# Kernel tuning notes

Hardware: AMD Instinct MI355X
Metric: run time of the kernel (lower is better)

Reference implementation:

```python
import jax, jax.numpy as jnp
import numpy as np

B, L, C = 2, 4096, 1024
H, WIN = 16, 128            # num_heads, window_size (each side)
D = C // H                  # head_dim = 64


def setup_inputs() -> dict:
    key = jax.random.key(0)
    ks = jax.random.split(key, 9)
    s = 0.02
    return {
        "x": jax.random.normal(ks[0], (B, L, C), jnp.float32),
        # Linear weights stored as [in, out] (y = x @ W + b), same math as torch Linear.
        "wq": jax.random.normal(ks[1], (C, C), jnp.float32) * s,
        "bq": jnp.zeros((C,), jnp.float32),
        "wk": jax.random.normal(ks[2], (C, C), jnp.float32) * s,
        "bk": jnp.zeros((C,), jnp.float32),
        "wv": jax.random.normal(ks[3], (C, C), jnp.float32) * s,
        "bv": jnp.zeros((C,), jnp.float32),
        "wo": jax.random.normal(ks[4], (C, C), jnp.float32) * s,
        "bo": jnp.zeros((C,), jnp.float32),
    }


def reference(x, wq, bq, wk, bk, wv, bv, wo, bo):
    b, l, c = x.shape
    nb = l // WIN

    def heads(t):  # (B,L,C) -> (B,H,L,D)
        return t.reshape(b, l, H, D).transpose(0, 2, 1, 3)

    q = heads(x @ wq + bq)
    k = heads(x @ wk + bk)
    v = heads(x @ wv + bv)

    # and ARE included in the softmax, exactly as the original module does).
    kp = jnp.pad(k, ((0, 0), (0, 0), (WIN, WIN), (0, 0)))
    vp = jnp.pad(v, ((0, 0), (0, 0), (WIN, WIN), (0, 0)))

    idx = np.arange(nb)[:, None] * WIN + np.arange(3 * WIN)[None, :]  # [nb, 3W]
    kb = kp[:, :, idx]  # [B,H,nb,3W,D]
    vb = vp[:, :, idx]  # [B,H,nb,3W,D]
    qb = q.reshape(b, H, nb, WIN, D)

    scores = jnp.einsum('bhnqd,bhnkd->bhnqk', qb, kb) / float(np.sqrt(D))
    r = np.arange(WIN)[:, None]
    col = np.arange(3 * WIN)[None, :]
    band = jnp.asarray(np.abs(col - r - WIN) <= WIN)
    scores = jnp.where(band, scores, -jnp.inf)
    probs = jax.nn.softmax(scores, axis=-1)

    out = jnp.einsum('bhnqk,bhnkd->bhnqd', probs, vb)
    out = out.reshape(b, H, l, D).transpose(0, 2, 1, 3).reshape(b, l, c)
    return out @ wo + bo
```

## Files before the change

### kernel.cpp

```cpp
#include <hip/hip_runtime.h>

using short8  = __attribute__((ext_vector_type(8))) short;
using short4v = __attribute__((ext_vector_type(4))) short;
using floatx4 = __attribute__((ext_vector_type(4))) float;

#define MFMA_B16(a, b, c) __builtin_amdgcn_mfma_f32_16x16x32_bf16(a, b, c, 0, 0, 0)

__device__ __forceinline__ short f2bf(float f) {
  union { float f; unsigned u; } v; v.f = f;
  unsigned r = v.u + 0x7fffu + ((v.u >> 16) & 1u);
  return (short)(r >> 16);
}

__device__ __forceinline__ void gload_lds16(const short* g, short* l) {
  __builtin_amdgcn_global_load_lds(
      (const __attribute__((address_space(1))) unsigned int*)g,
      (__attribute__((address_space(3))) unsigned int*)l, 16, 0, 0);
}

__global__ __launch_bounds__(256) void prep(
    const float4* __restrict__ x, short4v* __restrict__ xb,
    const float* __restrict__ w0, const float* __restrict__ w1,
    const float* __restrict__ w2, const float* __restrict__ w3,
    short* __restrict__ wT) {
  __shared__ float tile[32][33];
  int blk = blockIdx.x;
  if (blk < 8192) {
    int i = blk * 256 + threadIdx.x;
    float4 v = x[i];
    short4v o = { f2bf(v.x), f2bf(v.y), f2bf(v.z), f2bf(v.w) };
    xb[i] = o;
  } else {
    int r = blk - 8192;
    int z = r >> 10; r &= 1023;
    const float* w = z == 0 ? w0 : (z == 1 ? w1 : (z == 2 ? w2 : w3));
    short* out = wT + (size_t)z * 1024 * 1024;
    int n0 = (r & 31) * 32, k0 = (r >> 5) * 32;
    int tx = threadIdx.x & 31, ty = threadIdx.x >> 5;
#pragma unroll
    for (int i = 0; i < 4; ++i)
      tile[ty + i * 8][tx] = w[(size_t)(k0 + ty + i * 8) * 1024 + n0 + tx];
    __syncthreads();
#pragma unroll
    for (int i = 0; i < 4; ++i)
      out[(size_t)(n0 + ty + i * 8) * 1024 + k0 + tx] = f2bf(tile[tx][ty + i * 8]);
  }
}

__global__ __launch_bounds__(256) void gemm_qkv(
    const short* __restrict__ xb, const short* __restrict__ wT,
    const float* __restrict__ bq, const float* __restrict__ bk,
    const float* __restrict__ bv, short* __restrict__ qkv,
    short* __restrict__ vstage) {
  const int K = 1024;
  int z = blockIdx.z;
  const short* wt = wT + (size_t)z * 1024 * 1024;
  const float* bias = z == 0 ? bq : (z == 1 ? bk : bv);
  short* out = (z == 2) ? vstage : qkv + (size_t)z * 8192 * 1024;

  int m0 = blockIdx.x * 128, n0 = blockIdx.y * 128;
  __shared__ __align__(16) short a[128][32];
  __shared__ __align__(16) short bt[128][32];
  int tid = threadIdx.x;
  int w = tid >> 6, lane = tid & 63, quad = lane >> 4, l16 = lane & 15;
  int wm = (w >> 1) * 64, wn = (w & 1) * 64;
  floatx4 zf = {0.f, 0.f, 0.f, 0.f};
  floatx4 acc[4][4];
#pragma unroll
  for (int i = 0; i < 4; ++i)
#pragma unroll
    for (int j = 0; j < 4; ++j) acc[i][j] = zf;

  int rowL = lane >> 2;
  int segL = (lane & 3) * 8;
  const short* ga = xb + (size_t)(m0 + w * 32 + rowL) * K + segL;
  const short* gb = wt + (size_t)(n0 + w * 32 + rowL) * K + segL;
  short* la = &a[w * 32][0];
  short* lb = &bt[w * 32][0];

  for (int k0 = 0; k0 < K; k0 += 32) {
    __syncthreads();
    gload_lds16(ga + k0, la);
    gload_lds16(ga + (size_t)16 * K + k0, la + 16 * 32);
    gload_lds16(gb + k0, lb);
    gload_lds16(gb + (size_t)16 * K + k0, lb + 16 * 32);
    __syncthreads();
    short8 af[4], bf[4];
#pragma unroll
    for (int t = 0; t < 4; ++t) {
      af[t] = *(const short8*)(&a[wm + t * 16 + l16][quad * 8]);
      bf[t] = *(const short8*)(&bt[wn + t * 16 + l16][quad * 8]);
    }
#pragma unroll
    for (int i = 0; i < 4; ++i)
#pragma unroll
      for (int j = 0; j < 4; ++j)
        acc[i][j] = MFMA_B16(af[i], bf[j], acc[i][j]);
  }

  float qs = (z == 0) ? 0.125f : 1.0f;
#pragma unroll
  for (int i = 0; i < 4; ++i)
#pragma unroll
    for (int j = 0; j < 4; ++j)
#pragma unroll
      for (int rg = 0; rg < 4; ++rg) {
        int m = m0 + wm + i * 16 + quad * 4 + rg;
        int cc = n0 + wn + j * 16 + l16;
        float v = (acc[i][j][rg] + bias[cc]) * qs;
        int b = m >> 12, l = m & 4095;
        int hh = cc >> 6, d = cc & 63;
        out[((size_t)(b * 16 + hh) * 4096 + l) * 64 + d] = f2bf(v);
      }
}

__global__ __launch_bounds__(256) void transpose_v(const short* __restrict__ vin,
                                                   short* __restrict__ vout) {
  __shared__ __align__(16) short t[64][72];
  int bh = blockIdx.x >> 6;
  int l0 = (blockIdx.x & 63) * 64;
  const short* src = vin + ((size_t)bh * 4096 + l0) * 64;
  int tid = threadIdx.x;
  int row = tid >> 2, seg = (tid & 3) * 16;
  *(short8*)(&t[row][seg])     = *(const short8*)(src + row * 64 + seg);
  *(short8*)(&t[row][seg + 8]) = *(const short8*)(src + row * 64 + seg + 8);
  __syncthreads();
  short* dst = vout + (size_t)bh * 64 * 4096 + l0;
  short8 p0, p1;
#pragma unroll
  for (int j = 0; j < 8; ++j) { p0[j] = t[seg + j][row]; p1[j] = t[seg + 8 + j][row]; }
  *(short8*)(dst + (size_t)row * 4096 + seg)     = p0;
  *(short8*)(dst + (size_t)row * 4096 + seg + 8) = p1;
}

__global__ __launch_bounds__(256) void attn_kern(const short* __restrict__ qkv,
                                                 short* __restrict__ attnb) {
  const int L = 4096, H = 16;
  int n = blockIdx.x, h = blockIdx.y, b = blockIdx.z;
  const size_t hs = (size_t)L * 64;
  const short* Qp = qkv + (size_t)(b * H + h) * hs;
  const short* Kp = qkv + (size_t)8192 * 1024 + (size_t)(b * H + h) * hs;
  const short* Vt = qkv + (size_t)2 * 8192 * 1024 + (size_t)(b * H + h) * hs;

  __shared__ __align__(16) short kt[128][72];
  __shared__ __align__(16) short vt[64][136];
  __shared__ __align__(16) short pl[4][32][136];

  int tid = threadIdx.x, w = tid >> 6, lane = tid & 63, quad = lane >> 4, l16 = lane & 15;

  short8 onesf;
  {
    short ov = (l16 == 0) ? (short)0x3F80 : (short)0;
#pragma unroll
    for (int j = 0; j < 8; ++j) onesf[j] = ov;
  }

  short8 qf[2][2];
#pragma unroll
  for (int rt = 0; rt < 2; ++rt)
#pragma unroll
    for (int ks = 0; ks < 2; ++ks)
      qf[rt][ks] = *(const short8*)(Qp + (size_t)(n * 128 + w * 32 + rt * 16 + l16) * 64 + ks * 32 + quad * 8);

  floatx4 zf = {0.f, 0.f, 0.f, 0.f};
  floatx4 o[2][4];
  floatx4 osum[2];
#pragma unroll
  for (int i = 0; i < 2; ++i) {
    osum[i] = zf;
#pragma unroll
    for (int j = 0; j < 4; ++j) o[i][j] = zf;
  }

#pragma unroll
  for (int c = 0; c < 3; ++c) {
    int bk = n - 1 + c;
    bool inr = (c == 1) || (c == 0 ? (n > 0) : (n < 31));
    __syncthreads();
    if (inr) {
      const short* kc_ = Kp + (size_t)bk * 128 * 64;
      int kr = tid >> 2, ksg = (tid & 3) * 16;
#pragma unroll
      for (int p = 0; p < 2; ++p) {
        int r2 = p * 64 + kr;
        *(short8*)(&kt[r2][ksg])     = *(const short8*)(kc_ + r2 * 64 + ksg);
        *(short8*)(&kt[r2][ksg + 8]) = *(const short8*)(kc_ + r2 * 64 + ksg + 8);
      }
      const short* vc_ = Vt + (size_t)bk * 128;
      int vr = tid >> 2, vsg = (tid & 3) * 32;
#pragma unroll
      for (int q2 = 0; q2 < 4; ++q2)
        *(short8*)(&vt[vr][vsg + q2 * 8]) = *(const short8*)(vc_ + (size_t)vr * 4096 + vsg + q2 * 8);
    } else {
      short8 z8 = {0, 0, 0, 0, 0, 0, 0, 0};
      int kr = tid >> 2, ksg = (tid & 3) * 16;
#pragma unroll
      for (int p = 0; p < 2; ++p) {
        int r2 = p * 64 + kr;
        *(short8*)(&kt[r2][ksg])     = z8;
        *(short8*)(&kt[r2][ksg + 8]) = z8;
      }
      int vr = tid >> 2, vsg = (tid & 3) * 32;
#pragma unroll
      for (int q2 = 0; q2 < 4; ++q2) *(short8*)(&vt[vr][vsg + q2 * 8]) = z8;
    }
    __syncthreads();

    floatx4 s[2][8];
#pragma unroll
    for (int rt = 0; rt < 2; ++rt)
#pragma unroll
      for (int ct = 0; ct < 8; ++ct) s[rt][ct] = zf;
#pragma unroll
    for (int ct = 0; ct < 8; ++ct) {
      bool any = (c == 0) ? (ct >= w * 2) : (c == 2) ? (ct <= w * 2 + 1) : true;
      if (any) {
        short8 kf0 = *(const short8*)(&kt[ct * 16 + l16][quad * 8]);
        short8 kf1 = *(const short8*)(&kt[ct * 16 + l16][32 + quad * 8]);
#pragma unroll
        for (int rt = 0; rt < 2; ++rt) {
          bool valid = (c == 0) ? (ct >= w * 2 + rt) : (c == 2) ? (ct <= w * 2 + rt) : true;
          if (valid) {
            s[rt][ct] = MFMA_B16(qf[rt][0], kf0, s[rt][ct]);
            s[rt][ct] = MFMA_B16(qf[rt][1], kf1, s[rt][ct]);
          }
        }
      }
    }

#pragma unroll
    for (int rt = 0; rt < 2; ++rt) {
      int wrt = w * 2 + rt;
#pragma unroll
      for (int ct = 0; ct < 8; ++ct) {
        bool tileMasked = (c == 0) ? (ct < wrt) : (c == 2) ? (ct > wrt) : false;
        bool ksDead = (c == 0) ? (2 * (ct >> 1) + 1 < wrt)
                    : (c == 2) ? (2 * (ct >> 1) > wrt) : false;
        if (ksDead) continue;
        if (tileMasked) {
#pragma unroll
          for (int rg = 0; rg < 4; ++rg)
            pl[w][rt * 16 + quad * 4 + rg][ct * 16 + l16] = 0;
        } else {
#pragma unroll
          for (int rg = 0; rg < 4; ++rg) {
            int r = w * 32 + rt * 16 + quad * 4 + rg;
            int j = ct * 16 + l16;
            float p = __expf(s[rt][ct][rg]);
            if (c == 0) p = (j < r) ? 0.f : p;
            if (c == 2) p = (j > r) ? 0.f : p;
            pl[w][rt * 16 + quad * 4 + rg][ct * 16 + l16] = f2bf(p);
          }
        }
      }
    }

    __syncthreads();

#pragma unroll
    for (int ks = 0; ks < 4; ++ks) {
      bool anyrt = (c == 0) ? (2 * ks + 1 >= w * 2) : (c == 2) ? (2 * ks <= w * 2 + 1) : true;
      if (!anyrt) continue;
      short8 vf[4];
#pragma unroll
      for (int ct = 0; ct < 4; ++ct)
        vf[ct] = *(const short8*)(&vt[ct * 16 + l16][ks * 32 + quad * 8]);
#pragma unroll
      for (int rt = 0; rt < 2; ++rt) {
        int wrt = w * 2 + rt;
        bool ksDead = (c == 0) ? (2 * ks + 1 < wrt) : (c == 2) ? (2 * ks > wrt) : false;
        if (ksDead) continue;
        short8 pf = *(const short8*)(&pl[w][rt * 16 + l16][ks * 32 + quad * 8]);
#pragma unroll
        for (int ct = 0; ct < 4; ++ct) o[rt][ct] = MFMA_B16(pf, vf[ct], o[rt][ct]);
        osum[rt] = MFMA_B16(pf, onesf, osum[rt]);
      }
    }
  }

#pragma unroll
  for (int rt = 0; rt < 2; ++rt) {
#pragma unroll
    for (int rg = 0; rg < 4; ++rg) {
      float ssum = __shfl(osum[rt][rg], lane & 48);
      float inv = 1.f / ssum;
      int r = n * 128 + w * 32 + rt * 16 + quad * 4 + rg;
#pragma unroll
      for (int ct = 0; ct < 4; ++ct)
        attnb[(size_t)(b * L + r) * 1024 + h * 64 + ct * 16 + l16] =
            f2bf(o[rt][ct][rg] * inv);
    }
  }
}

__global__ __launch_bounds__(256) void gemm_out(
    const short* __restrict__ attnb, const short* __restrict__ wTo,
    const float* __restrict__ bo, float* __restrict__ outp) {
  const int K = 1024;
  int m0 = blockIdx.x * 128, n0 = blockIdx.y * 128;
  __shared__ __align__(16) short a[128][32];
  __shared__ __align__(16) short bt[128][32];
  int tid = threadIdx.x;
  int w = tid >> 6, lane = tid & 63, quad = lane >> 4, l16 = lane & 15;
  int wm = (w >> 1) * 64, wn = (w & 1) * 64;
  floatx4 zf = {0.f, 0.f, 0.f, 0.f};
  floatx4 acc[4][4];
#pragma unroll
  for (int i = 0; i < 4; ++i)
#pragma unroll
    for (int j = 0; j < 4; ++j) acc[i][j] = zf;

  int rowL = lane >> 2;
  int segL = (lane & 3) * 8;
  const short* ga = attnb + (size_t)(m0 + w * 32 + rowL) * K + segL;
  const short* gb = wTo + (size_t)(n0 + w * 32 + rowL) * K + segL;
  short* la = &a[w * 32][0];
  short* lb = &bt[w * 32][0];

  for (int k0 = 0; k0 < K; k0 += 32) {
    __syncthreads();
    gload_lds16(ga + k0, la);
    gload_lds16(ga + (size_t)16 * K + k0, la + 16 * 32);
    gload_lds16(gb + k0, lb);
    gload_lds16(gb + (size_t)16 * K + k0, lb + 16 * 32);
    __syncthreads();
    short8 af[4], bf[4];
#pragma unroll
    for (int t = 0; t < 4; ++t) {
      af[t] = *(const short8*)(&a[wm + t * 16 + l16][quad * 8]);
      bf[t] = *(const short8*)(&bt[wn + t * 16 + l16][quad * 8]);
    }
#pragma unroll
    for (int i = 0; i < 4; ++i)
#pragma unroll
      for (int j = 0; j < 4; ++j)
        acc[i][j] = MFMA_B16(af[i], bf[j], acc[i][j]);
  }
#pragma unroll
  for (int i = 0; i < 4; ++i)
#pragma unroll
    for (int j = 0; j < 4; ++j)
#pragma unroll
      for (int rg = 0; rg < 4; ++rg) {
        int m = m0 + wm + i * 16 + quad * 4 + rg;
        int c = n0 + wn + j * 16 + l16;
        outp[(size_t)m * 1024 + c] = acc[i][j][rg] + bo[c];
      }
}

extern "C" void kernel_launch(void* const* d_in, const int* in_sizes, int n_in,
                              void* d_out, int out_size, void* d_ws, size_t ws_size,
                              hipStream_t stream) {
  const float* x  = (const float*)d_in[0];
  const float* wq = (const float*)d_in[1];
  const float* bq = (const float*)d_in[2];
  const float* wk = (const float*)d_in[3];
  const float* bk = (const float*)d_in[4];
  const float* wv = (const float*)d_in[5];
  const float* bv = (const float*)d_in[6];
  const float* wo = (const float*)d_in[7];
  const float* bo = (const float*)d_in[8];

  char* ws = (char*)d_ws;
  short* xb     = (short*)ws;
  short* wT     = (short*)(ws + (16u << 20));
  short* qkv    = (short*)(ws + (24u << 20));
  short* attnb  = (short*)(ws + (72u << 20));
  short* vstage = attnb;

  prep<<<12288, 256, 0, stream>>>((const float4*)x, (short4v*)xb, wq, wk, wv, wo, wT);
  gemm_qkv<<<dim3(64, 8, 3), 256, 0, stream>>>(xb, wT, bq, bk, bv, qkv, vstage);
  transpose_v<<<2048, 256, 0, stream>>>(vstage, qkv + (size_t)2 * 8192 * 1024);
  attn_kern<<<dim3(32, 16, 2), 256, 0, stream>>>(qkv, attnb);
  gemm_out<<<dim3(64, 8), 256, 0, stream>>>(attnb, wT + 3u * 1024 * 1024, bo, (float*)d_out);
}
```

Measured before the change: 229.0 us.

## Load attention K/V fragments from global directly, use exp2 scaling, shrink out-GEMM tile

The attention kernel stops staging K and V tiles in shared memory. Each wave now reads its MFMA fragments straight from global memory, which removes two barriers per chunk and frees LDS. Log2(e) is folded into the Q scale so the kernel can call exp2f, and probabilities are truncated to bf16 instead of rounded. The output GEMM uses 64-row tiles to launch twice as many blocks, trading data reuse per block for more parallelism; the uncoalesced fragment loads and the truncation rounding are the risks.

New measurement: 258.1 us. 1.13x slower.

```diff
diff --git a/kernel.cpp b/kernel.cpp
--- a/kernel.cpp
+++ b/kernel.cpp
@@ -10,6 +10,10 @@
   union { float f; unsigned u; } v; v.f = f;
   unsigned r = v.u + 0x7fffu + ((v.u >> 16) & 1u);
   return (short)(r >> 16);
+}
+__device__ __forceinline__ short f2bf_rtz(float f) {
+  union { float f; unsigned u; } v; v.f = f;
+  return (short)(v.u >> 16);
 }
 
 __device__ __forceinline__ void gload_lds16(const short* g, short* l) {
@@ -98,7 +102,7 @@
         acc[i][j] = MFMA_B16(af[i], bf[j], acc[i][j]);
   }
 
-  float qs = (z == 0) ? 0.125f : 1.0f;
+  float qs = (z == 0) ? 0.125f * 1.44269504f : 1.0f;
 #pragma unroll
   for (int i = 0; i < 4; ++i)
 #pragma unroll
@@ -142,12 +146,11 @@
   const short* Kp = qkv + (size_t)8192 * 1024 + (size_t)(b * H + h) * hs;
   const short* Vt = qkv + (size_t)2 * 8192 * 1024 + (size_t)(b * H + h) * hs;
 
-  __shared__ __align__(16) short kt[128][72];
-  __shared__ __align__(16) short vt[64][136];
   __shared__ __align__(16) short pl[4][32][136];
 
   int tid = threadIdx.x, w = tid >> 6, lane = tid & 63, quad = lane >> 4, l16 = lane & 15;
 
+  short8 z8 = {0, 0, 0, 0, 0, 0, 0, 0};
   short8 onesf;
   {
     short ov = (l16 == 0) ? (short)0x3F80 : (short)0;
@@ -176,57 +179,34 @@
   for (int c = 0; c < 3; ++c) {
     int bk = n - 1 + c;
     bool inr = (c == 1) || (c == 0 ? (n > 0) : (n < 31));
-    __syncthreads();
+
+    floatx4 s[2][8];
+#pragma unroll
+    for (int rt = 0; rt < 2; ++rt)
+#pragma unroll
+      for (int ct = 0; ct < 8; ++ct) s[rt][ct] = zf;
     if (inr) {
       const short* kc_ = Kp + (size_t)bk * 128 * 64;
-      int kr = tid >> 2, ksg = (tid & 3) * 16;
-#pragma unroll
-      for (int p = 0; p < 2; ++p) {
-        int r2 = p * 64 + kr;
-        *(short8*)(&kt[r2][ksg])     = *(const short8*)(kc_ + r2 * 64 + ksg);
-        *(short8*)(&kt[r2][ksg + 8]) = *(const short8*)(kc_ + r2 * 64 + ksg + 8);
-      }
-      const short* vc_ = Vt + (size_t)bk * 128;
-      int vr = tid >> 2, vsg = (tid & 3) * 32;
-#pragma unroll
-      for (int q2 = 0; q2 < 4; ++q2)
-        *(short8*)(&vt[vr][vsg + q2 * 8]) = *(const short8*)(vc_ + (size_t)vr * 4096 + vsg + q2 * 8);
-    } else {
-      short8 z8 = {0, 0, 0, 0, 0, 0, 0, 0};
-      int kr = tid >> 2, ksg = (tid & 3) * 16;
-#pragma unroll
-      for (int p = 0; p < 2; ++p) {
-        int r2 = p * 64 + kr;
-        *(short8*)(&kt[r2][ksg])     = z8;
-        *(short8*)(&kt[r2][ksg + 8]) = z8;
-      }
-      int vr = tid >> 2, vsg = (tid & 3) * 32;
-#pragma unroll
-      for (int q2 = 0; q2 < 4; ++q2) *(short8*)(&vt[vr][vsg + q2 * 8]) = z8;
-    }
-    __syncthreads();
-
-    floatx4 s[2][8];
-#pragma unroll
-    for (int rt = 0; rt < 2; ++rt)
-#pragma unroll
-      for (int ct = 0; ct < 8; ++ct) s[rt][ct] = zf;
-#pragma unroll
-    for (int ct = 0; ct < 8; ++ct) {
-      bool any = (c == 0) ? (ct >= w * 2) : (c == 2) ? (ct <= w * 2 + 1) : true;
-      if (any) {
-        short8 kf0 = *(const short8*)(&kt[ct * 16 + l16][quad * 8]);
-        short8 kf1 = *(const short8*)(&kt[ct * 16 + l16][32 + quad * 8]);
-#pragma unroll
-        for (int rt = 0; rt < 2; ++rt) {
-          bool valid = (c == 0) ? (ct >= w * 2 + rt) : (c == 2) ? (ct <= w * 2 + rt) : true;
-          if (valid) {
-            s[rt][ct] = MFMA_B16(qf[rt][0], kf0, s[rt][ct]);
-            s[rt][ct] = MFMA_B16(qf[rt][1], kf1, s[rt][ct]);
+#pragma unroll
+      for (int ct = 0; ct < 8; ++ct) {
+        bool any = (c == 0) ? (ct >= w * 2) : (c == 2) ? (ct <= w * 2 + 1) : true;
+        if (any) {
+          const short* kr_ = kc_ + (ct * 16 + l16) * 64 + quad * 8;
+          short8 kf0 = *(const short8*)(kr_);
+          short8 kf1 = *(const short8*)(kr_ + 32);
+#pragma unroll
+          for (int rt = 0; rt < 2; ++rt) {
+            bool valid = (c == 0) ? (ct >= w * 2 + rt) : (c == 2) ? (ct <= w * 2 + rt) : true;
+            if (valid) {
+              s[rt][ct] = MFMA_B16(qf[rt][0], kf0, s[rt][ct]);
+              s[rt][ct] = MFMA_B16(qf[rt][1], kf1, s[rt][ct]);
+            }
           }
         }
       }
     }
+
+    if (c > 0) __syncthreads();
 
 #pragma unroll
     for (int rt = 0; rt < 2; ++rt) {
@@ -246,10 +226,10 @@
           for (int rg = 0; rg < 4; ++rg) {
             int r = w * 32 + rt * 16 + quad * 4 + rg;
             int j = ct * 16 + l16;
-            float p = __expf(s[rt][ct][rg]);
+            float p = exp2f(s[rt][ct][rg]);
             if (c == 0) p = (j < r) ? 0.f : p;
             if (c == 2) p = (j > r) ? 0.f : p;
-            pl[w][rt * 16 + quad * 4 + rg][ct * 16 + l16] = f2bf(p);
+            pl[w][rt * 16 + quad * 4 + rg][ct * 16 + l16] = f2bf_rtz(p);
           }
         }
       }
@@ -257,6 +237,7 @@
 
     __syncthreads();
 
+    const short* vc_ = Vt + (size_t)bk * 128;
 #pragma unroll
     for (int ks = 0; ks < 4; ++ks) {
       bool anyrt = (c == 0) ? (2 * ks + 1 >= w * 2) : (c == 2) ? (2 * ks <= w * 2 + 1) : true;
@@ -264,7 +245,8 @@
       short8 vf[4];
 #pragma unroll
       for (int ct = 0; ct < 4; ++ct)
-        vf[ct] = *(const short8*)(&vt[ct * 16 + l16][ks * 32 + quad * 8]);
+        vf[ct] = inr ? *(const short8*)(vc_ + (size_t)(ct * 16 + l16) * 4096 + ks * 32 + quad * 8)
+                     : z8;
 #pragma unroll
       for (int rt = 0; rt < 2; ++rt) {
         int wrt = w * 2 + rt;
@@ -297,47 +279,47 @@
     const short* __restrict__ attnb, const short* __restrict__ wTo,
     const float* __restrict__ bo, float* __restrict__ outp) {
   const int K = 1024;
-  int m0 = blockIdx.x * 128, n0 = blockIdx.y * 128;
-  __shared__ __align__(16) short a[128][32];
+  int m0 = blockIdx.x * 64, n0 = blockIdx.y * 128;
+  __shared__ __align__(16) short a[64][32];
   __shared__ __align__(16) short bt[128][32];
   int tid = threadIdx.x;
   int w = tid >> 6, lane = tid & 63, quad = lane >> 4, l16 = lane & 15;
-  int wm = (w >> 1) * 64, wn = (w & 1) * 64;
+  int wm = (w >> 1) * 32, wn = (w & 1) * 64;
   floatx4 zf = {0.f, 0.f, 0.f, 0.f};
-  floatx4 acc[4][4];
-#pragma unroll
-  for (int i = 0; i < 4; ++i)
+  floatx4 acc[2][4];
+#pragma unroll
+  for (int i = 0; i < 2; ++i)
 #pragma unroll
     for (int j = 0; j < 4; ++j) acc[i][j] = zf;
 
   int rowL = lane >> 2;
   int segL = (lane & 3) * 8;
-  const short* ga = attnb + (size_t)(m0 + w * 32 + rowL) * K + segL;
+  const short* ga = attnb + (size_t)(m0 + w * 16 + rowL) * K + segL;
   const short* gb = wTo + (size_t)(n0 + w * 32 + rowL) * K + segL;
-  short* la = &a[w * 32][0];
+  short* la = &a[w * 16][0];
   short* lb = &bt[w * 32][0];
 
   for (int k0 = 0; k0 < K; k0 += 32) {
     __syncthreads();
     gload_lds16(ga + k0, la);
-    gload_lds16(ga + (size_t)16 * K + k0, la + 16 * 32);
     gload_lds16(gb + k0, lb);
     gload_lds16(gb + (size_t)16 * K + k0, lb + 16 * 32);
     __syncthreads();
-    short8 af[4], bf[4];
-#pragma unroll
-    for (int t = 0; t < 4; ++t) {
+    short8 af[2], bf[4];
+#pragma unroll
+    for (int t = 0; t < 2; ++t)
       af[t] = *(const short8*)(&a[wm + t * 16 + l16][quad * 8]);
+#pragma unroll
+    for (int t = 0; t < 4; ++t)
       bf[t] = *(const short8*)(&bt[wn + t * 16 + l16][quad * 8]);
-    }
-#pragma unroll
-    for (int i = 0; i < 4; ++i)
+#pragma unroll
+    for (int i = 0; i < 2; ++i)
 #pragma unroll
       for (int j = 0; j < 4; ++j)
         acc[i][j] = MFMA_B16(af[i], bf[j], acc[i][j]);
   }
 #pragma unroll
-  for (int i = 0; i < 4; ++i)
+  for (int i = 0; i < 2; ++i)
 #pragma unroll
     for (int j = 0; j < 4; ++j)
 #pragma unroll
@@ -372,5 +354,5 @@
   gemm_qkv<<<dim3(64, 8, 3), 256, 0, stream>>>(xb, wT, bq, bk, bv, qkv, vstage);
   transpose_v<<<2048, 256, 0, stream>>>(vstage, qkv + (size_t)2 * 8192 * 1024);
   attn_kern<<<dim3(32, 16, 2), 256, 0, stream>>>(qkv, attnb);
-  gemm_out<<<dim3(64, 8), 256, 0, stream>>>(attnb, wT + 3u * 1024 * 1024, bo, (float*)d_out);
-}
+  gemm_out<<<dim3(128, 8), 256, 0, stream>>>(attnb, wT + 3u * 1024 * 1024, bo, (float*)d_out);
+}
```

## Drop V transpose kernel, widen QKV GEMM K-tile, use exp2 with prescaled Q

Applied to the files above, without the earlier changes.

Removes the separate transpose_v kernel. The attention kernel now loads V in row-major layout and transposes it into shared memory as it stores, which saves one launch and a full round trip of V through global memory. The QKV GEMM stages 64-wide K tiles instead of 32, halving the number of barrier pairs per output tile. Q is prescaled by log2(e) so the softmax can use exp2f, and probabilities are truncated to bf16 instead of rounded. The scalar transposed LDS stores may cause bank conflicts, and truncation adds a small bias to precision.

Measured after the change: 242.2 us. +5.8%, slower.

```diff
diff --git a/kernel.cpp b/kernel.cpp
--- a/kernel.cpp
+++ b/kernel.cpp
@@ -10,6 +10,10 @@
   union { float f; unsigned u; } v; v.f = f;
   unsigned r = v.u + 0x7fffu + ((v.u >> 16) & 1u);
   return (short)(r >> 16);
+}
+__device__ __forceinline__ short f2bf_rtz(float f) {
+  union { float f; unsigned u; } v; v.f = f;
+  return (short)(v.u >> 16);
 }
 
 __device__ __forceinline__ void gload_lds16(const short* g, short* l) {
@@ -50,17 +54,16 @@
 __global__ __launch_bounds__(256) void gemm_qkv(
     const short* __restrict__ xb, const short* __restrict__ wT,
     const float* __restrict__ bq, const float* __restrict__ bk,
-    const float* __restrict__ bv, short* __restrict__ qkv,
-    short* __restrict__ vstage) {
+    const float* __restrict__ bv, short* __restrict__ qkv) {
   const int K = 1024;
   int z = blockIdx.z;
   const short* wt = wT + (size_t)z * 1024 * 1024;
   const float* bias = z == 0 ? bq : (z == 1 ? bk : bv);
-  short* out = (z == 2) ? vstage : qkv + (size_t)z * 8192 * 1024;
+  short* out = qkv + (size_t)z * 8192 * 1024;
 
   int m0 = blockIdx.x * 128, n0 = blockIdx.y * 128;
-  __shared__ __align__(16) short a[128][32];
-  __shared__ __align__(16) short bt[128][32];
+  __shared__ __align__(16) short a[128][64];
+  __shared__ __align__(16) short bt[128][64];
   int tid = threadIdx.x;
   int w = tid >> 6, lane = tid & 63, quad = lane >> 4, l16 = lane & 15;
   int wm = (w >> 1) * 64, wn = (w & 1) * 64;
@@ -71,34 +74,38 @@
 #pragma unroll
     for (int j = 0; j < 4; ++j) acc[i][j] = zf;
 
-  int rowL = lane >> 2;
-  int segL = (lane & 3) * 8;
+  int rowL = lane >> 3;
+  int segL = (lane & 7) * 8;
   const short* ga = xb + (size_t)(m0 + w * 32 + rowL) * K + segL;
   const short* gb = wt + (size_t)(n0 + w * 32 + rowL) * K + segL;
   short* la = &a[w * 32][0];
   short* lb = &bt[w * 32][0];
 
-  for (int k0 = 0; k0 < K; k0 += 32) {
-    __syncthreads();
-    gload_lds16(ga + k0, la);
-    gload_lds16(ga + (size_t)16 * K + k0, la + 16 * 32);
-    gload_lds16(gb + k0, lb);
-    gload_lds16(gb + (size_t)16 * K + k0, lb + 16 * 32);
-    __syncthreads();
-    short8 af[4], bf[4];
-#pragma unroll
-    for (int t = 0; t < 4; ++t) {
-      af[t] = *(const short8*)(&a[wm + t * 16 + l16][quad * 8]);
-      bf[t] = *(const short8*)(&bt[wn + t * 16 + l16][quad * 8]);
-    }
-#pragma unroll
-    for (int i = 0; i < 4; ++i)
-#pragma unroll
-      for (int j = 0; j < 4; ++j)
-        acc[i][j] = MFMA_B16(af[i], bf[j], acc[i][j]);
-  }
-
-  float qs = (z == 0) ? 0.125f : 1.0f;
+  for (int k0 = 0; k0 < K; k0 += 64) {
+    __syncthreads();
+#pragma unroll
+    for (int cc = 0; cc < 4; ++cc) {
+      gload_lds16(ga + (size_t)(cc * 8) * K + k0, la + cc * 8 * 64);
+      gload_lds16(gb + (size_t)(cc * 8) * K + k0, lb + cc * 8 * 64);
+    }
+    __syncthreads();
+#pragma unroll
+    for (int kk = 0; kk < 2; ++kk) {
+      short8 af[4], bf[4];
+#pragma unroll
+      for (int t = 0; t < 4; ++t) {
+        af[t] = *(const short8*)(&a[wm + t * 16 + l16][kk * 32 + quad * 8]);
+        bf[t] = *(const short8*)(&bt[wn + t * 16 + l16][kk * 32 + quad * 8]);
+      }
+#pragma unroll
+      for (int i = 0; i < 4; ++i)
+#pragma unroll
+        for (int j = 0; j < 4; ++j)
+          acc[i][j] = MFMA_B16(af[i], bf[j], acc[i][j]);
+    }
+  }
+
+  float qs = (z == 0) ? 0.125f * 1.44269504f : 1.0f;
 #pragma unroll
   for (int i = 0; i < 4; ++i)
 #pragma unroll
@@ -114,25 +121,6 @@
       }
 }
 
-__global__ __launch_bounds__(256) void transpose_v(const short* __restrict__ vin,
-                                                   short* __restrict__ vout) {
-  __shared__ __align__(16) short t[64][72];
-  int bh = blockIdx.x >> 6;
-  int l0 = (blockIdx.x & 63) * 64;
-  const short* src = vin + ((size_t)bh * 4096 + l0) * 64;
-  int tid = threadIdx.x;
-  int row = tid >> 2, seg = (tid & 3) * 16;
-  *(short8*)(&t[row][seg])     = *(const short8*)(src + row * 64 + seg);
-  *(short8*)(&t[row][seg + 8]) = *(const short8*)(src + row * 64 + seg + 8);
-  __syncthreads();
-  short* dst = vout + (size_t)bh * 64 * 4096 + l0;
-  short8 p0, p1;
-#pragma unroll
-  for (int j = 0; j < 8; ++j) { p0[j] = t[seg + j][row]; p1[j] = t[seg + 8 + j][row]; }
-  *(short8*)(dst + (size_t)row * 4096 + seg)     = p0;
-  *(short8*)(dst + (size_t)row * 4096 + seg + 8) = p1;
-}
-
 __global__ __launch_bounds__(256) void attn_kern(const short* __restrict__ qkv,
                                                  short* __restrict__ attnb) {
   const int L = 4096, H = 16;
@@ -140,7 +128,7 @@
   const size_t hs = (size_t)L * 64;
   const short* Qp = qkv + (size_t)(b * H + h) * hs;
   const short* Kp = qkv + (size_t)8192 * 1024 + (size_t)(b * H + h) * hs;
-  const short* Vt = qkv + (size_t)2 * 8192 * 1024 + (size_t)(b * H + h) * hs;
+  const short* Vp = qkv + (size_t)2 * 8192 * 1024 + (size_t)(b * H + h) * hs;
 
   __shared__ __align__(16) short kt[128][72];
   __shared__ __align__(16) short vt[64][136];
@@ -186,11 +174,15 @@
         *(short8*)(&kt[r2][ksg])     = *(const short8*)(kc_ + r2 * 64 + ksg);
         *(short8*)(&kt[r2][ksg + 8]) = *(const short8*)(kc_ + r2 * 64 + ksg + 8);
       }
-      const short* vc_ = Vt + (size_t)bk * 128;
-      int vr = tid >> 2, vsg = (tid & 3) * 32;
-#pragma unroll
-      for (int q2 = 0; q2 < 4; ++q2)
-        *(short8*)(&vt[vr][vsg + q2 * 8]) = *(const short8*)(vc_ + (size_t)vr * 4096 + vsg + q2 * 8);
+      const short* vc_ = Vp + (size_t)bk * 128 * 64;
+      int vkey = tid & 31, vsg = (tid >> 5) * 8;
+#pragma unroll
+      for (int p = 0; p < 4; ++p) {
+        int r2 = p * 32 + vkey;
+        short8 vv = *(const short8*)(vc_ + r2 * 64 + vsg);
+#pragma unroll
+        for (int j = 0; j < 8; ++j) vt[vsg + j][r2] = vv[j];
+      }
     } else {
       short8 z8 = {0, 0, 0, 0, 0, 0, 0, 0};
       int kr = tid >> 2, ksg = (tid & 3) * 16;
@@ -200,9 +192,9 @@
         *(short8*)(&kt[r2][ksg])     = z8;
         *(short8*)(&kt[r2][ksg + 8]) = z8;
       }
-      int vr = tid >> 2, vsg = (tid & 3) * 32;
-#pragma unroll
-      for (int q2 = 0; q2 < 4; ++q2) *(short8*)(&vt[vr][vsg + q2 * 8]) = z8;
+      int vr = tid >> 2, vsg2 = (tid & 3) * 32;
+#pragma unroll
+      for (int q2 = 0; q2 < 4; ++q2) *(short8*)(&vt[vr][vsg2 + q2 * 8]) = z8;
     }
     __syncthreads();
 
@@ -246,10 +238,10 @@
           for (int rg = 0; rg < 4; ++rg) {
             int r = w * 32 + rt * 16 + quad * 4 + rg;
             int j = ct * 16 + l16;
-            float p = __expf(s[rt][ct][rg]);
+            float p = exp2f(s[rt][ct][rg]);
             if (c == 0) p = (j < r) ? 0.f : p;
             if (c == 2) p = (j > r) ? 0.f : p;
-            pl[w][rt * 16 + quad * 4 + rg][ct * 16 + l16] = f2bf(p);
+            pl[w][rt * 16 + quad * 4 + rg][ct * 16 + l16] = f2bf_rtz(p);
           }
         }
       }
@@ -362,15 +354,13 @@
   const float* bo = (const float*)d_in[8];
 
   char* ws = (char*)d_ws;
-  short* xb     = (short*)ws;
-  short* wT     = (short*)(ws + (16u << 20));
-  short* qkv    = (short*)(ws + (24u << 20));
-  short* attnb  = (short*)(ws + (72u << 20));
-  short* vstage = attnb;
+  short* xb    = (short*)ws;
+  short* wT    = (short*)(ws + (16u << 20));
+  short* qkv   = (short*)(ws + (24u << 20));
+  short* attnb = (short*)(ws + (72u << 20));
 
   prep<<<12288, 256, 0, stream>>>((const float4*)x, (short4v*)xb, wq, wk, wv, wo, wT);
-  gemm_qkv<<<dim3(64, 8, 3), 256, 0, stream>>>(xb, wT, bq, bk, bv, qkv, vstage);
-  transpose_v<<<2048, 256, 0, stream>>>(vstage, qkv + (size_t)2 * 8192 * 1024);
+  gemm_qkv<<<dim3(64, 8, 3), 256, 0, stream>>>(xb, wT, bq, bk, bv, qkv);
   attn_kern<<<dim3(32, 16, 2), 256, 0, stream>>>(qkv, attnb);
   gemm_out<<<dim3(64, 8), 256, 0, stream>>>(attnb, wT + 3u * 1024 * 1024, bo, (float*)d_out);
 }
```
